# Kernel optimization log

Hardware: AMD Instinct MI355X
Metric: run time of the kernel (lower is better)

Reference implementation:

```python
import jax, jax.numpy as jnp
import numpy as np

WIN = 9  # local window size per spatial dim

def _boxfilter3d(x):
    k = jnp.ones((1, 1, WIN, WIN, WIN), x.dtype) / float(WIN ** 3)
    return jax.lax.conv_general_dilated(
        x, k, window_strides=(1, 1, 1), padding='SAME',
        dimension_numbers=('NCDHW', 'OIDHW', 'NCDHW'))

def setup_inputs() -> dict:
    key = jax.random.key(0)
    k1, k2 = jax.random.split(key)
    shape = (2, 1, 160, 192, 160)
    y_true = jax.random.uniform(k1, shape, dtype=jnp.float32)
    y_pred = jax.random.uniform(k2, shape, dtype=jnp.float32)
    return {"y_true": y_true, "y_pred": y_pred}

def reference(y_true, y_pred):
    Ii, Ji = y_true, y_pred
    mu1 = _boxfilter3d(Ii)
    mu2 = _boxfilter3d(Ji)
    sigma1_sq = _boxfilter3d(Ii * Ii) - mu1 * mu1
    sigma2_sq = _boxfilter3d(Ji * Ji) - mu2 * mu2
    sigma12 = _boxfilter3d(Ii * Ji) - mu1 * mu2
    cc = (sigma12 * sigma12) / (sigma1_sq * sigma2_sq + 1e-5)
    return -jnp.mean(cc)
```

## Files before the change

kernel.cpp:

```cpp
#include <hip/hip_runtime.h>

#define DD 160
#define HH 192
#define WW 160
#define HWs (HH * WW)
#define NTOT 9830400.0f
#define DOUT 20
#define NIT  28
#define NBLK 960

#define SDS 11
#define SDC (24 * SDS)
#define HSS 11
#define HSC (16 * HSS)

typedef float    v4 __attribute__((ext_vector_type(4)));
typedef _Float16 h4 __attribute__((ext_vector_type(4)));

__device__ __forceinline__ void block_sync_lds() {
    __builtin_amdgcn_s_waitcnt(0xc07f);
    __builtin_amdgcn_s_barrier();
}
__device__ __forceinline__ v4 up(h4 x) { return __builtin_convertvector(x, v4); }
__device__ __forceinline__ h4 dn(v4 x) { return __builtin_convertvector(x, h4); }

__global__ __launch_bounds__(256, 4) void kf(const float* __restrict__ I,
                                             const float* __restrict__ J,
                                             float* __restrict__ partial) {
    __shared__ h4    SDL[5 * SDC];
    __shared__ h4    HSL[5 * HSC];
    __shared__ float red[128];

    const int tid = threadIdx.x;
    const int bx = blockIdx.x, by = blockIdx.y, b = blockIdx.z;
    const int w0 = (bx % 5) * 32, h0 = (bx / 5) * 16;
    const int d0 = by * DOUT;
    const int bid = bx + 60 * (by + 8 * b);

    const bool p1 = tid < 240;
    const int r = tid / 10, g = tid % 10;
    const int gh = h0 - 4 + r, gw = w0 - 4 + g * 4;
    const bool colOK = p1 && gh >= 0 && gh < HH && gw >= 0 && gw < WW;
    const size_t colOff = (size_t)gh * WW + gw;
    const float* Ib = I + (size_t)b * DD * HWs + colOff;
    const float* Jb = J + (size_t)b * DD * HWs + colOff;
    h4* const sdw = &SDL[r * SDS + g];

    const bool p2 = tid < 100;
    const int g2 = tid % 10, q2 = tid / 10;
    const int ch2 = q2 >> 1, hh0 = (q2 & 1) * 8;
    const h4* const sdr = &SDL[ch2 * SDC + hh0 * SDS + g2];
    h4* const hsw = &HSL[ch2 * HSC + hh0 * HSS + g2];

    const bool p3 = tid < 128;
    const int hh = tid >> 3, sg = tid & 7;
    const h4* const hsr = &HSL[hh * HSS + sg];

    v4 sd0 = 0.f, sd1 = 0.f, sd2 = 0.f, sd3 = 0.f, sd4 = 0.f;
    h4 fI[9], fJ[9];
#pragma unroll
    for (int u = 0; u < 9; ++u) { fI[u] = (h4)(_Float16)0; fJ[u] = (h4)(_Float16)0; }
    v4 pLI = 0.f, pLJ = 0.f;
    float acc = 0.f;
    const float inv = 1.0f / 729.0f;

    {
        const int si = d0 - 4;
        if (colOK && si >= 0) {
            pLI = *(const v4*)(Ib + (size_t)si * HWs);
            pLJ = *(const v4*)(Jb + (size_t)si * HWs);
        }
    }

    for (int tb = 0; tb < NIT; tb += 9) {
#pragma unroll
        for (int u = 0; u < 9; ++u) {
            const int t = tb + u;
            if (t < NIT) {
                const int si = d0 - 4 + t;
                if (p1) {
                    h4 cI = dn(pLI), cJ = dn(pLJ);
                    v4 aI = up(cI), aJ = up(cJ);
                    v4 dI = aI, dJv = aJ;
                    v4 dII = aI * aI, dJJ = aJ * aJ, dIJ = aI * aJ;
                    if (t >= 9) {
                        v4 bI = up(fI[u]), bJ = up(fJ[u]);
                        dI -= bI; dJv -= bJ;
                        dII -= bI * bI; dJJ -= bJ * bJ; dIJ -= bI * bJ;
                    }
                    fI[u] = cI; fJ[u] = cJ;
                    sd0 += dI; sd1 += dJv; sd2 += dII; sd3 += dJJ; sd4 += dIJ;
                    sdw[0]       = dn(sd0);
                    sdw[SDC]     = dn(sd1);
                    sdw[2 * SDC] = dn(sd2);
                    sdw[3 * SDC] = dn(sd3);
                    sdw[4 * SDC] = dn(sd4);
                    pLI = 0.f; pLJ = 0.f;
                    const int sn = si + 1;
                    if (t + 1 < NIT && colOK && sn >= 0 && sn < DD) {
                        pLI = *(const v4*)(Ib + (size_t)sn * HWs);
                        pLJ = *(const v4*)(Jb + (size_t)sn * HWs);
                    }
                }
                block_sync_lds();
                if (p2) {
                    v4 s = 0.f;
#pragma unroll
                    for (int k = 0; k < 9; ++k) s += up(sdr[k * SDS]);
                    hsw[0] = dn(s);
#pragma unroll
                    for (int j2 = 1; j2 < 8; ++j2) {
                        s += up(sdr[(j2 + 8) * SDS]) - up(sdr[(j2 - 1) * SDS]);
                        hsw[j2 * HSS] = dn(s);
                    }
                }
                block_sync_lds();
                if (p3 && t >= 8) {
                    float w[5][4];
#pragma unroll
                    for (int c = 0; c < 5; ++c) {
                        v4 fa = up(hsr[c * HSC]);
                        v4 fb = up(hsr[c * HSC + 1]);
                        v4 fc = up(hsr[c * HSC + 2]);
                        float s = fa[0] + fa[1] + fa[2] + fa[3] +
                                  fb[0] + fb[1] + fb[2] + fb[3] + fc[0];
                        w[c][0] = s;
                        s += fc[1] - fa[0]; w[c][1] = s;
                        s += fc[2] - fa[1]; w[c][2] = s;
                        s += fc[3] - fa[2]; w[c][3] = s;
                    }
#pragma unroll
                    for (int e = 0; e < 4; ++e) {
                        float mu1 = w[0][e] * inv, mu2 = w[1][e] * inv;
                        float g1  = fmaf(-mu1, mu1, w[2][e] * inv);
                        float g2v = fmaf(-mu2, mu2, w[3][e] * inv);
                        float g12 = fmaf(-mu1, mu2, w[4][e] * inv);
                        acc += __fdividef(g12 * g12, fmaf(g1, g2v, 1e-5f));
                    }
                }
            }
        }
    }

    if (p3) red[tid] = acc;
    __syncthreads();
    if (tid < 64) {
        float a = red[tid] + red[tid + 64];
#pragma unroll
        for (int off = 32; off > 0; off >>= 1) a += __shfl_down(a, off);
        if (tid == 0) partial[bid] = a;
    }
}

__global__ void k3_final(const float* __restrict__ partial,
                         float* __restrict__ out) {
    __shared__ float r[1024];
    const int i = threadIdx.x;
    r[i] = (i < NBLK) ? partial[i] : 0.f;
    __syncthreads();
    for (int off = 512; off > 0; off >>= 1) {
        if (i < off) r[i] += r[i + off];
        __syncthreads();
    }
    if (i == 0) out[0] = -r[0] * (1.0f / NTOT);
}

extern "C" void kernel_launch(void* const* d_in, const int* in_sizes, int n_in,
                              void* d_out, int out_size, void* d_ws, size_t ws_size,
                              hipStream_t stream) {
    (void)in_sizes; (void)n_in; (void)out_size; (void)ws_size;
    const float* I = (const float*)d_in[0];
    const float* J = (const float*)d_in[1];
    float* out     = (float*)d_out;
    float* partial = (float*)d_ws;

    dim3 grid(60, 8, 2);
    kf<<<grid, 256, 0, stream>>>(I, J, partial);
    k3_final<<<1, 1024, 0, stream>>>(partial, out);
}
```

Measured before the change: 153.3 us.

## Software-pipeline box-filter stages with double-buffered LDS and one barrier per step

The depth, height and width stages now run as a three-stage software pipeline over double-buffered LDS, so each depth step needs one barrier instead of two and the stages work on different slices at once. The loop runs two extra iterations to drain the pipeline. Thread roles are remapped with an XOR on block index so the stage-2 and stage-3 threads land in different wavefronts across blocks. Stage 2 now accumulates in fp16 rather than fp32, which saves conversions but may lose precision. LDS padding is added to reduce bank conflicts, at the cost of more LDS per block.

```diff
diff --git a/kernel.cpp b/kernel.cpp
--- a/kernel.cpp
+++ b/kernel.cpp
@@ -10,9 +10,11 @@
 #define NBLK 960
 
 #define SDS 11
-#define SDC (24 * SDS)
+#define SDC (24 * SDS + 1)
+#define SDP (5 * SDC)
 #define HSS 11
-#define HSC (16 * HSS)
+#define HSC (16 * HSS + 1)
+#define HSP (5 * HSC)
 
 typedef float    v4 __attribute__((ext_vector_type(4)));
 typedef _Float16 h4 __attribute__((ext_vector_type(4)));
@@ -27,9 +29,9 @@
 __global__ __launch_bounds__(256, 4) void kf(const float* __restrict__ I,
                                              const float* __restrict__ J,
                                              float* __restrict__ partial) {
-    __shared__ h4    SDL[5 * SDC];
-    __shared__ h4    HSL[5 * HSC];
-    __shared__ float red[128];
+    __shared__ h4    SDL[2 * SDP];
+    __shared__ h4    HSL[2 * HSP];
+    __shared__ float red[256];
 
     const int tid = threadIdx.x;
     const int bx = blockIdx.x, by = blockIdx.y, b = blockIdx.z;
@@ -37,8 +39,10 @@
     const int d0 = by * DOUT;
     const int bid = bx + 60 * (by + 8 * b);
 
-    const bool p1 = tid < 240;
-    const int r = tid / 10, g = tid % 10;
+    const int rt = tid ^ ((bx & 1) << 7);
+
+    const bool p1 = rt < 240;
+    const int r = rt / 10, g = rt % 10;
     const int gh = h0 - 4 + r, gw = w0 - 4 + g * 4;
     const bool colOK = p1 && gh >= 0 && gh < HH && gw >= 0 && gw < WW;
     const size_t colOff = (size_t)gh * WW + gw;
@@ -46,15 +50,15 @@
     const float* Jb = J + (size_t)b * DD * HWs + colOff;
     h4* const sdw = &SDL[r * SDS + g];
 
-    const bool p2 = tid < 100;
-    const int g2 = tid % 10, q2 = tid / 10;
-    const int ch2 = q2 >> 1, hh0 = (q2 & 1) * 8;
-    const h4* const sdr = &SDL[ch2 * SDC + hh0 * SDS + g2];
-    h4* const hsw = &HSL[ch2 * HSC + hh0 * HSS + g2];
+    const bool p2 = rt < 100;
+    const int g2 = rt % 10, ch2 = (rt / 10) % 5, hh0 = (rt / 50) * 8;
+    const int sdrOff = ch2 * SDC + hh0 * SDS + g2;
+    const int hswOff = ch2 * HSC + hh0 * HSS + g2;
 
-    const bool p3 = tid < 128;
-    const int hh = tid >> 3, sg = tid & 7;
-    const h4* const hsr = &HSL[hh * HSS + sg];
+    const bool p3 = rt >= 128;
+    const int q3 = rt & 127;
+    const int hh = q3 >> 3, sg = q3 & 7;
+    const int hsrOff = hh * HSS + sg;
 
     v4 sd0 = 0.f, sd1 = 0.f, sd2 = 0.f, sd3 = 0.f, sd4 = 0.f;
     h4 fI[9], fJ[9];
@@ -72,13 +76,12 @@
         }
     }
 
-    for (int tb = 0; tb < NIT; tb += 9) {
+    for (int tb = 0; tb < 36; tb += 9) {
 #pragma unroll
         for (int u = 0; u < 9; ++u) {
             const int t = tb + u;
-            if (t < NIT) {
-                const int si = d0 - 4 + t;
-                if (p1) {
+            if (t < NIT + 2) {
+                if (t < NIT && p1) {
                     h4 cI = dn(pLI), cJ = dn(pLJ);
                     v4 aI = up(cI), aJ = up(cJ);
                     v4 dI = aI, dJv = aJ;
@@ -90,32 +93,37 @@
                     }
                     fI[u] = cI; fJ[u] = cJ;
                     sd0 += dI; sd1 += dJv; sd2 += dII; sd3 += dJJ; sd4 += dIJ;
-                    sdw[0]       = dn(sd0);
-                    sdw[SDC]     = dn(sd1);
-                    sdw[2 * SDC] = dn(sd2);
-                    sdw[3 * SDC] = dn(sd3);
-                    sdw[4 * SDC] = dn(sd4);
+                    h4* const sdq = sdw + (t & 1) * SDP;
+                    sdq[0]       = dn(sd0);
+                    sdq[SDC]     = dn(sd1);
+                    sdq[2 * SDC] = dn(sd2);
+                    sdq[3 * SDC] = dn(sd3);
+                    sdq[4 * SDC] = dn(sd4);
                     pLI = 0.f; pLJ = 0.f;
-                    const int sn = si + 1;
+                    const int sn = d0 - 3 + t;
                     if (t + 1 < NIT && colOK && sn >= 0 && sn < DD) {
                         pLI = *(const v4*)(Ib + (size_t)sn * HWs);
                         pLJ = *(const v4*)(Jb + (size_t)sn * HWs);
                     }
                 }
-                block_sync_lds();
-                if (p2) {
-                    v4 s = 0.f;
+
+                if (t >= 1 && t <= NIT && p2) {
+                    const int par = (t - 1) & 1;
+                    const h4* const sdr = &SDL[par * SDP + sdrOff];
+                    h4* const hsw = &HSL[par * HSP + hswOff];
+                    h4 s = sdr[0];
 #pragma unroll
-                    for (int k = 0; k < 9; ++k) s += up(sdr[k * SDS]);
-                    hsw[0] = dn(s);
+                    for (int k = 1; k < 9; ++k) s += sdr[k * SDS];
+                    hsw[0] = s;
 #pragma unroll
-                    for (int j2 = 1; j2 < 8; ++j2) {
-                        s += up(sdr[(j2 + 8) * SDS]) - up(sdr[(j2 - 1) * SDS]);
-                        hsw[j2 * HSS] = dn(s);
+                    for (int j = 1; j < 8; ++j) {
+                        s += sdr[(j + 8) * SDS] - sdr[(j - 1) * SDS];
+                        hsw[j * HSS] = s;
                     }
                 }
-                block_sync_lds();
-                if (p3 && t >= 8) {
+
+                if (t >= 10 && p3) {
+                    const h4* const hsr = &HSL[(t & 1) * HSP + hsrOff];
                     float w[5][4];
 #pragma unroll
                     for (int c = 0; c < 5; ++c) {
@@ -138,11 +146,15 @@
                         acc += __fdividef(g12 * g12, fmaf(g1, g2v, 1e-5f));
                     }
                 }
+
+                block_sync_lds();
             }
         }
     }
 
-    if (p3) red[tid] = acc;
+    red[tid] = acc;
+    __syncthreads();
+    if (tid < 128) red[tid] += red[tid + 128];
     __syncthreads();
     if (tid < 64) {
         float a = red[tid] + red[tid + 64];
```

New measurement: 148.3 us. 3.2% less time.
